# Performance work log

Hardware: AMD Instinct MI355X
Metric: run time of the kernel (lower is better)

The kernel has to match this reference:

```python
import jax, jax.numpy as jnp
import numpy as np

EPS = 1e-5

def layer_norm(x, g, b):
    mu = jnp.mean(x, axis=-1, keepdims=True)
    var = jnp.mean(jnp.square(x - mu), axis=-1, keepdims=True)
    return (x - mu) * jax.lax.rsqrt(var + EPS) * g + b

def setup_inputs() -> dict:
    key = jax.random.key(0)
    ks = jax.random.split(key, 8)
    B, N, C, H = 1, 384, 128, 128
    s = 0.02
    return {
        "pair": jax.random.normal(ks[0], (B, N, N, C), dtype=jnp.float32),
        "ln_l_g": jnp.ones((C,), jnp.float32), "ln_l_b": jnp.zeros((C,), jnp.float32),
        "ln_r_g": jnp.ones((C,), jnp.float32), "ln_r_b": jnp.zeros((C,), jnp.float32),
        "Wl": jax.random.normal(ks[1], (C, H), jnp.float32) * s, "bl": jnp.zeros((H,), jnp.float32),
        "Wr": jax.random.normal(ks[2], (C, H), jnp.float32) * s, "br": jnp.zeros((H,), jnp.float32),
        "Wg": jax.random.normal(ks[3], (C, H), jnp.float32) * s, "bg": jnp.zeros((H,), jnp.float32),
        "Wo": jax.random.normal(ks[4], (H, C), jnp.float32) * s, "bo": jnp.zeros((C,), jnp.float32),
        "n_g": jnp.ones((C,), jnp.float32), "n_b": jnp.zeros((C,), jnp.float32),
    }

def reference(pair, ln_l_g, ln_l_b, ln_r_g, ln_r_b, Wl, bl, Wr, br, Wg, bg, Wo, bo, n_g, n_b):
    # pair: [B, N, N, C]
    left = layer_norm(pair, ln_l_g, ln_l_b) @ Wl + bl      # [B,N,N,H]
    right = layer_norm(pair, ln_r_g, ln_r_b) @ Wr + br     # [B,N,N,H]
    gate = jax.nn.sigmoid(pair @ Wg + bg)                  # [B,N,N,H]
    # triangle multiplicative update: per-channel N x N matmul over k
    out = jnp.einsum('bikh,bkjh->bijh', left, right)
    out = out * gate
    out = out @ Wo + bo                                    # [B,N,N,C]
    return layer_norm(out + pair, n_g, n_b)
```

## Files before the change

### kernel.cpp

```cpp
#include <hip/hip_runtime.h>
#include <hip/hip_bf16.h>

#define N_ 384
#define C_ 128
#define M_ (N_*N_)

typedef __attribute__((ext_vector_type(8))) short bf16x8_t;
typedef __attribute__((ext_vector_type(4))) float f32x4_t;
typedef unsigned int u32;
typedef unsigned short u16;
typedef unsigned long long u64;

__device__ __forceinline__ u16 f2bf(float f) {
  u32 u = __builtin_bit_cast(u32, f);
  u32 r = (u + 0x7FFFu + ((u >> 16) & 1u)) >> 16;
  return (u16)r;
}
__device__ __forceinline__ float bf2f(u16 h) {
  u32 u = ((u32)h) << 16;
  return __builtin_bit_cast(float, u);
}

__global__ __launch_bounds__(256) void k_prep(const float* __restrict__ lg, const float* __restrict__ rg,
    const float* __restrict__ Wl, const float* __restrict__ Wr, const float* __restrict__ Wg,
    const float* __restrict__ Wo,
    const float* __restrict__ lb, const float* __restrict__ rb,
    const float* __restrict__ bl, const float* __restrict__ br, const float* __restrict__ bg,
    u16* __restrict__ wcat, u16* __restrict__ wot,
    float* __restrict__ bcat, float* __restrict__ sg) {
  int bx = blockIdx.x, t = threadIdx.x;
  if (bx < 256) {
    int idx = bx*256 + t;
    if (idx < 49152) {
      int n = idx >> 7, k = idx & 127;
      float v;
      if (n < 128)      v = lg[k] * Wl[k*128 + n];
      else if (n < 256) v = rg[k] * Wr[k*128 + (n-128)];
      else              v = Wg[k*128 + (n-256)];
      wcat[idx] = f2bf(v);
    } else {
      int i2 = idx - 49152;
      int c = i2 >> 7, h = i2 & 127;
      wot[i2] = f2bf(Wo[h*128 + c]);
    }
  } else if (bx == 256) {
    float s = 0.f;
    if (t < 128)      { for (int k=0;k<128;k++) s += lb[k]*Wl[k*128+t];       s += bl[t];     bcat[t] = s; }
    else              { int hh=t-128; for (int k=0;k<128;k++) s += rb[k]*Wr[k*128+hh]; s += br[hh]; bcat[t] = s; }
  } else {
    if (t < 128)      { bcat[256+t] = bg[t]; }
    else              { int hh = t-128; float s=0.f; for (int k=0;k<128;k++) s += Wg[k*128+hh]; sg[hh] = s; }
  }
}

#define LDK 136
#define LDA 72
#define LDW 72
#define LDT 136

__global__ __launch_bounds__(512) void k_projln(const float* __restrict__ pair,
    const u16* __restrict__ wcat, const float* __restrict__ bcat, const float* __restrict__ sg,
    u16* __restrict__ left_t, u16* __restrict__ right_t, u16* __restrict__ gate_t) {
  __shared__ u16 At[128*LDK];
  __shared__ float mu_s[128];
  __shared__ float irs_s[128];
  int bx = blockIdx.x;
  int r0 = bx * 128;
  int t = threadIdx.x, w = t>>6, lane = t&63;
  int q = lane>>4, nl = lane&15;

  {
    int rr = t >> 2, quarter = t & 3;
    const float4* gp = (const float4*)(pair + (size_t)(r0+rr)*128 + quarter*32);
    float4 v[8];
    #pragma unroll
    for (int i=0;i<8;i++) v[i] = gp[i];
    float s=0.f, qq=0.f;
    #pragma unroll
    for (int i=0;i<8;i++) {
      s  += v[i].x + v[i].y + v[i].z + v[i].w;
      qq += v[i].x*v[i].x + v[i].y*v[i].y + v[i].z*v[i].z + v[i].w*v[i].w;
    }
    s  += __shfl_xor(s, 1, 64);
    s  += __shfl_xor(s, 2, 64);
    qq += __shfl_xor(qq, 1, 64);
    qq += __shfl_xor(qq, 2, 64);
    float mu = s * (1.f/128.f);
    float var = qq*(1.f/128.f) - mu*mu;
    float rstd = rsqrtf(var + 1e-5f);
    if (quarter == 0) { mu_s[rr] = mu; irs_s[rr] = 1.0f/rstd; }
    u32* lp = (u32*)(At + rr*LDK + quarter*32);
    #pragma unroll
    for (int i=0;i<4;i++) {
      u32 p0 = (u32)f2bf((v[2*i].x-mu)*rstd)   | ((u32)f2bf((v[2*i].y-mu)*rstd)<<16);
      u32 p1 = (u32)f2bf((v[2*i].z-mu)*rstd)   | ((u32)f2bf((v[2*i].w-mu)*rstd)<<16);
      u32 p2 = (u32)f2bf((v[2*i+1].x-mu)*rstd) | ((u32)f2bf((v[2*i+1].y-mu)*rstd)<<16);
      u32 p3 = (u32)f2bf((v[2*i+1].z-mu)*rstd) | ((u32)f2bf((v[2*i+1].w-mu)*rstd)<<16);
      ((uint4*)lp)[i] = make_uint4(p0,p1,p2,p3);
    }
  }
  __syncthreads();

  #pragma unroll 1
  for (int nb = 0; nb < 3; ++nb) {
    const u16* bbase = wcat + (size_t)(nb*128)*128;
    f32x4_t acc[8] = {};
    #pragma unroll
    for (int ks=0; ks<4; ks++) {
      int kel = ks*32 + q*8;
      bf16x8_t b = *(const bf16x8_t*)(bbase + (size_t)(w*16 + nl)*128 + kel);
      #pragma unroll
      for (int tm=0;tm<8;tm++) {
        bf16x8_t a = *(const bf16x8_t*)(At + (tm*16+nl)*LDK + kel);
        acc[tm] = __builtin_amdgcn_mfma_f32_16x16x32_bf16(a, b, acc[tm], 0,0,0);
      }
    }
    u16* dst = (nb==0) ? left_t : (nb==1) ? right_t : gate_t;
    int n = w*16 + nl;
    float bias = bcat[nb*128 + n];
    u16* rowp = dst + (size_t)n*M_ + r0;
    if (nb == 2) {
      float sgn = sg[n];
      #pragma unroll
      for (int tm=0;tm<8;tm++) {
        f32x4_t mu4 = *(const f32x4_t*)(mu_s  + tm*16 + q*4);
        f32x4_t ir4 = *(const f32x4_t*)(irs_s + tm*16 + q*4);
        float v0 = acc[tm][0]*ir4[0] + mu4[0]*sgn + bias;
        float v1 = acc[tm][1]*ir4[1] + mu4[1]*sgn + bias;
        float v2 = acc[tm][2]*ir4[2] + mu4[2]*sgn + bias;
        float v3 = acc[tm][3]*ir4[3] + mu4[3]*sgn + bias;
        v0 = 1.0f/(1.0f+__expf(-v0));
        v1 = 1.0f/(1.0f+__expf(-v1));
        v2 = 1.0f/(1.0f+__expf(-v2));
        v3 = 1.0f/(1.0f+__expf(-v3));
        u32 pk0 = (u32)f2bf(v0) | ((u32)f2bf(v1)<<16);
        u32 pk1 = (u32)f2bf(v2) | ((u32)f2bf(v3)<<16);
        *(u64*)(rowp + tm*16 + q*4) = (u64)pk0 | ((u64)pk1<<32);
      }
    } else {
      #pragma unroll
      for (int tm=0;tm<8;tm++) {
        u32 pk0 = (u32)f2bf(acc[tm][0]+bias) | ((u32)f2bf(acc[tm][1]+bias)<<16);
        u32 pk1 = (u32)f2bf(acc[tm][2]+bias) | ((u32)f2bf(acc[tm][3]+bias)<<16);
        *(u64*)(rowp + tm*16 + q*4) = (u64)pk0 | ((u64)pk1<<32);
      }
    }
  }
}

__global__ __launch_bounds__(512) void k_einsum(const u16* __restrict__ left_t, const u16* __restrict__ right_t,
    const u16* __restrict__ gate_t, u16* __restrict__ og_t) {
  __shared__ u16 smem[2*128*LDA];
  u16* At = smem; u16* Bt = smem + 128*LDA;
  int bx = blockIdx.x;
  int wk = (bx & 7) * 144 + (bx >> 3);
  int h = wk / 9; int rem = wk % 9;
  int i0 = (rem/3)*128, j0 = (rem%3)*128;
  const u16* Ag = left_t + (size_t)h*M_;
  const u16* Bg = right_t + (size_t)h*M_;
  int t = threadIdx.x, w = t>>6, lane = t&63;
  int q = lane>>4, nl = lane&15;
  f32x4_t acc[4][2] = {};
  int m0 = (w&1)*64, nb0 = (w>>1)*32;
  for (int kb = 0; kb < N_; kb += 64) {
    {
      int rr = t>>2, quarter = t&3;
      const u16* gp = Ag + (size_t)(i0+rr)*N_ + kb + quarter*16;
      u16* lp = At + rr*LDA + quarter*16;
      ((uint4*)lp)[0] = ((const uint4*)gp)[0];
      ((uint4*)lp)[1] = ((const uint4*)gp)[1];
    }
    {
      int kk2 = t>>4;
      int seg = t&15;
      const u16* g0 = Bg + (size_t)(kb + 2*kk2)*N_ + j0 + seg*8;
      const u16* g1 = g0 + N_;
      uint4 ra = ((const uint4*)g0)[0];
      uint4 rbv = ((const uint4*)g1)[0];
      u32 w0[4] = {ra.x,ra.y,ra.z,ra.w};
      u32 w1[4] = {rbv.x,rbv.y,rbv.z,rbv.w};
      u32 sw = (u32)(seg>>1) << 4;
      char* bbytes = (char*)Bt;
      #pragma unroll
      for (int e=0;e<4;e++) {
        u32 lo = w0[e], hi = w1[e];
        u32 evenw = (lo & 0xffffu) | (hi << 16);
        u32 oddw  = (lo >> 16)     | (hi & 0xffff0000u);
        int je = seg*8 + 2*e;
        u32 byteE = ((u32)(je*LDA + 2*kk2) * 2u) ^ sw;
        u32 byteO = ((u32)((je+1)*LDA + 2*kk2) * 2u) ^ sw;
        *(u32*)(bbytes + byteE) = evenw;
        *(u32*)(bbytes + byteO) = oddw;
      }
    }
    __syncthreads();
    #pragma unroll
    for (int ks=0; ks<2; ks++) {
      int kel = ks*32 + q*8;
      bf16x8_t a[4], b[2];
      #pragma unroll
      for (int tm=0;tm<4;tm++) a[tm] = *(const bf16x8_t*)(At + (m0+tm*16+nl)*LDA + kel);
      #pragma unroll
      for (int tn=0;tn<2;tn++) {
        u32 swr = (u32)(((nb0>>4) + tn) & 7) << 4;
        b[tn] = *(const bf16x8_t*)((const char*)Bt + ((u32)(((nb0+tn*16+nl)*LDA + kel)*2) ^ swr));
      }
      #pragma unroll
      for (int tm=0;tm<4;tm++)
        #pragma unroll
        for (int tn=0;tn<2;tn++)
          acc[tm][tn] = __builtin_amdgcn_mfma_f32_16x16x32_bf16(a[tm], b[tn], acc[tm][tn], 0,0,0);
    }
    __syncthreads();
  }
  u16* Ot = smem;
  #pragma unroll
  for (int tm=0;tm<4;tm++)
    #pragma unroll
    for (int tn=0;tn<2;tn++)
      #pragma unroll
      for (int p=0;p<4;p++) {
        int m = m0 + tm*16 + q*4 + p;
        int n = nb0 + tn*16 + nl;
        Ot[m*LDT + n] = f2bf(acc[tm][tn][p]);
      }
  __syncthreads();
  {
    int m = t>>2, hq = t&3;
    size_t rbase = (size_t)h*M_ + (size_t)(i0+m)*N_ + j0 + hq*32;
    const uint4* gg = (const uint4*)(gate_t + rbase);
    const uint4* lo = (const uint4*)(Ot + m*LDT + hq*32);
    uint4* od = (uint4*)(og_t + rbase);
    #pragma unroll
    for (int i=0;i<4;i++) {
      uint4 gv = gg[i]; uint4 ov = lo[i];
      u32 ga[4] = {gv.x,gv.y,gv.z,gv.w};
      u32 oa[4] = {ov.x,ov.y,ov.z,ov.w};
      u32 ra2[4];
      #pragma unroll
      for (int e=0;e<4;e++) {
        float g0 = bf2f((u16)(ga[e]&0xffffu)), g1 = bf2f((u16)(ga[e]>>16));
        float o0 = bf2f((u16)(oa[e]&0xffffu)), o1 = bf2f((u16)(oa[e]>>16));
        ra2[e] = (u32)f2bf(o0*g0) | ((u32)f2bf(o1*g1)<<16);
      }
      od[i] = make_uint4(ra2[0],ra2[1],ra2[2],ra2[3]);
    }
  }
}

__global__ __launch_bounds__(512) void k_final(const u16* __restrict__ og_t, const u16* __restrict__ wot,
    const float* __restrict__ pair, const float* __restrict__ bo,
    const float* __restrict__ ng, const float* __restrict__ nb_,
    float* __restrict__ out) {
  __shared__ u16 smem[2*128*LDW];
  u16* At = smem; u16* Wt = smem + 128*LDW;
  int bx = blockIdx.x;
  int r0 = bx * 128;
  int t = threadIdx.x, w = t>>6, lane = t&63;
  int q = lane>>4, nl = lane&15;
  f32x4_t acc[8] = {};
  int m0 = w*16;
  for (int c0 = 0; c0 < 128; c0 += 64) {
    {
      int hh = t>>3, seg = t&7;
      const u16* gp = og_t + (size_t)(c0+hh)*M_ + r0 + seg*16;
      uint4 b0 = ((const uint4*)gp)[0];
      uint4 b1 = ((const uint4*)gp)[1];
      u32 xs[8] = {b0.x,b0.y,b0.z,b0.w,b1.x,b1.y,b1.z,b1.w};
      #pragma unroll
      for (int e=0;e<8;e++) {
        int rb = seg*16 + 2*e;
        At[(rb+0)*LDW+hh] = (u16)(xs[e]&0xffffu);
        At[(rb+1)*LDW+hh] = (u16)(xs[e]>>16);
      }
    }
    {
      int c = t>>2, q4 = t&3;
      const u16* gp = wot + (size_t)c*128 + c0 + q4*16;
      u16* lp = Wt + c*LDW + q4*16;
      ((uint4*)lp)[0] = ((const uint4*)gp)[0];
      ((uint4*)lp)[1] = ((const uint4*)gp)[1];
    }
    __syncthreads();
    #pragma unroll
    for (int ks=0; ks<2; ks++) {
      int kel = ks*32 + q*8;
      bf16x8_t a = *(const bf16x8_t*)(At + (m0+nl)*LDW + kel);
      bf16x8_t b[8];
      #pragma unroll
      for (int tn=0;tn<8;tn++) b[tn] = *(const bf16x8_t*)(Wt + (tn*16+nl)*LDW + kel);
      #pragma unroll
      for (int tn=0;tn<8;tn++)
        acc[tn] = __builtin_amdgcn_mfma_f32_16x16x32_bf16(a, b[tn], acc[tn], 0,0,0);
    }
    __syncthreads();
  }
  float rsum[4], rsq[4];
  #pragma unroll
  for (int p=0;p<4;p++) { rsum[p]=0.f; rsq[p]=0.f; }
  #pragma unroll
  for (int tn=0;tn<8;tn++) {
    int n = tn*16 + nl;
    float bb = bo[n];
    #pragma unroll
    for (int p=0;p<4;p++) {
      int m = m0 + q*4 + p;
      float v = acc[tn][p] + bb + pair[(size_t)(r0+m)*128 + n];
      acc[tn][p] = v;
      rsum[p] += v;
      rsq[p]  += v*v;
    }
  }
  #pragma unroll
  for (int msk=1; msk<16; msk<<=1) {
    #pragma unroll
    for (int p=0;p<4;p++) {
      rsum[p] += __shfl_xor(rsum[p], msk, 64);
      rsq[p]  += __shfl_xor(rsq[p],  msk, 64);
    }
  }
  #pragma unroll
  for (int p=0;p<4;p++) {
    float mu = rsum[p] * (1.f/128.f);
    float var = rsq[p]*(1.f/128.f) - mu*mu;
    rsum[p] = mu;
    rsq[p] = rsqrtf(var + 1e-5f);
  }
  #pragma unroll
  for (int tn=0;tn<8;tn++) {
    int n = tn*16 + nl;
    float g = ng[n], b2 = nb_[n];
    #pragma unroll
    for (int p=0;p<4;p++) {
      int m = m0 + q*4 + p;
      out[(size_t)(r0+m)*128 + n] = (acc[tn][p] - rsum[p]) * rsq[p] * g + b2;
    }
  }
}

extern "C" void kernel_launch(void* const* d_in, const int* in_sizes, int n_in,
                              void* d_out, int out_size, void* d_ws, size_t ws_size,
                              hipStream_t stream) {
  (void)in_sizes; (void)n_in; (void)out_size; (void)ws_size;
  const float* pair   = (const float*)d_in[0];
  const float* ln_l_g = (const float*)d_in[1];
  const float* ln_l_b = (const float*)d_in[2];
  const float* ln_r_g = (const float*)d_in[3];
  const float* ln_r_b = (const float*)d_in[4];
  const float* Wl = (const float*)d_in[5];
  const float* bl = (const float*)d_in[6];
  const float* Wr = (const float*)d_in[7];
  const float* br = (const float*)d_in[8];
  const float* Wg = (const float*)d_in[9];
  const float* bg = (const float*)d_in[10];
  const float* Wo = (const float*)d_in[11];
  const float* bo = (const float*)d_in[12];
  const float* n_g = (const float*)d_in[13];
  const float* n_b = (const float*)d_in[14];

  char* ws = (char*)d_ws;
  const size_t SZ = (size_t)M_*128*sizeof(u16);
  u16*  og_t    = (u16*)(ws);
  u16*  gate_t  = (u16*)(ws + SZ);
  u16*  wcat    = (u16*)(ws + 2*SZ);
  float* bcat   = (float*)(ws + 2*SZ + 98304);
  float* sgp    = (float*)(ws + 2*SZ + 98304 + 1536);
  u16*  wot     = (u16*)(ws + 2*SZ + 98304 + 1536 + 512);

  u16* left_t   = (u16*)d_out;
  u16* right_t  = (u16*)d_out + (size_t)M_*128;

  k_prep<<<258, 256, 0, stream>>>(ln_l_g, ln_r_g, Wl, Wr, Wg, Wo,
                                  ln_l_b, ln_r_b, bl, br, bg, wcat, wot, bcat, sgp);
  k_projln<<<1152, 512, 0, stream>>>(pair, wcat, bcat, sgp, left_t, right_t, gate_t);
  k_einsum<<<1152, 512, 0, stream>>>(left_t, right_t, gate_t, og_t);
  k_final<<<1152, 512, 0, stream>>>(og_t, wot, pair, bo, n_g, n_b, (float*)d_out);
}
```

Baseline: 271.4 us.

## Store intermediates as 128x128 tiles so each block's writes and reads are contiguous

Left/right, gate and gated-output intermediates change from a channel-major [H][N*N] layout to a tiled layout. Left and right blocks of one 128-row tile are interleaved together, and each 128-row by 128-channel tile is stored contiguously. Projection and final kernels now write and read one contiguous 32KB region per block instead of 128 strided rows spread across M. The einsum kernel reads 256-byte segments from scattered tiles instead of contiguous rows, so its access locality may suffer.

```diff
diff --git a/kernel.cpp b/kernel.cpp
--- a/kernel.cpp
+++ b/kernel.cpp
@@ -60,7 +60,7 @@
 
 __global__ __launch_bounds__(512) void k_projln(const float* __restrict__ pair,
     const u16* __restrict__ wcat, const float* __restrict__ bcat, const float* __restrict__ sg,
-    u16* __restrict__ left_t, u16* __restrict__ right_t, u16* __restrict__ gate_t) {
+    u16* __restrict__ lr_, u16* __restrict__ gate_) {
   __shared__ u16 At[128*LDK];
   __shared__ float mu_s[128];
   __shared__ float irs_s[128];
@@ -115,10 +115,12 @@
         acc[tm] = __builtin_amdgcn_mfma_f32_16x16x32_bf16(a, b, acc[tm], 0,0,0);
       }
     }
-    u16* dst = (nb==0) ? left_t : (nb==1) ? right_t : gate_t;
     int n = w*16 + nl;
     float bias = bcat[nb*128 + n];
-    u16* rowp = dst + (size_t)n*M_ + r0;
+    u16* rowp;
+    if (nb == 0)      rowp = lr_   + ((size_t)bx*256 + n)*128;
+    else if (nb == 1) rowp = lr_   + ((size_t)bx*256 + 128 + n)*128;
+    else              rowp = gate_ + ((size_t)bx*128 + n)*128;
     if (nb == 2) {
       float sgn = sg[n];
       #pragma unroll
@@ -148,24 +150,23 @@
   }
 }
 
-__global__ __launch_bounds__(512) void k_einsum(const u16* __restrict__ left_t, const u16* __restrict__ right_t,
-    const u16* __restrict__ gate_t, u16* __restrict__ og_t) {
+__global__ __launch_bounds__(512) void k_einsum(const u16* __restrict__ lr_,
+    const u16* __restrict__ gate_, u16* __restrict__ og_) {
   __shared__ u16 smem[2*128*LDA];
   u16* At = smem; u16* Bt = smem + 128*LDA;
   int bx = blockIdx.x;
   int wk = (bx & 7) * 144 + (bx >> 3);
   int h = wk / 9; int rem = wk % 9;
-  int i0 = (rem/3)*128, j0 = (rem%3)*128;
-  const u16* Ag = left_t + (size_t)h*M_;
-  const u16* Bg = right_t + (size_t)h*M_;
+  int i0 = (rem/3)*128, j0c = rem%3;
   int t = threadIdx.x, w = t>>6, lane = t&63;
   int q = lane>>4, nl = lane&15;
   f32x4_t acc[4][2] = {};
   int m0 = (w&1)*64, nb0 = (w>>1)*32;
   for (int kb = 0; kb < N_; kb += 64) {
+    int c = kb >> 7, off = kb & 127;
     {
       int rr = t>>2, quarter = t&3;
-      const u16* gp = Ag + (size_t)(i0+rr)*N_ + kb + quarter*16;
+      const u16* gp = lr_ + (((size_t)(i0+rr)*3 + c)*256 + h)*128 + off + quarter*16;
       u16* lp = At + rr*LDA + quarter*16;
       ((uint4*)lp)[0] = ((const uint4*)gp)[0];
       ((uint4*)lp)[1] = ((const uint4*)gp)[1];
@@ -173,8 +174,8 @@
     {
       int kk2 = t>>4;
       int seg = t&15;
-      const u16* g0 = Bg + (size_t)(kb + 2*kk2)*N_ + j0 + seg*8;
-      const u16* g1 = g0 + N_;
+      const u16* g0 = lr_ + (((size_t)(kb + 2*kk2)*3 + j0c)*256 + 128 + h)*128 + seg*8;
+      const u16* g1 = g0 + 3*256*128;
       uint4 ra = ((const uint4*)g0)[0];
       uint4 rbv = ((const uint4*)g1)[0];
       u32 w0[4] = {ra.x,ra.y,ra.z,ra.w};
@@ -227,10 +228,10 @@
   __syncthreads();
   {
     int m = t>>2, hq = t&3;
-    size_t rbase = (size_t)h*M_ + (size_t)(i0+m)*N_ + j0 + hq*32;
-    const uint4* gg = (const uint4*)(gate_t + rbase);
+    size_t gbase = (((size_t)(i0+m)*3 + j0c)*128 + h)*128 + hq*32;
+    const uint4* gg = (const uint4*)(gate_ + gbase);
     const uint4* lo = (const uint4*)(Ot + m*LDT + hq*32);
-    uint4* od = (uint4*)(og_t + rbase);
+    uint4* od = (uint4*)(og_ + gbase);
     #pragma unroll
     for (int i=0;i<4;i++) {
       uint4 gv = gg[i]; uint4 ov = lo[i];
@@ -248,7 +249,7 @@
   }
 }
 
-__global__ __launch_bounds__(512) void k_final(const u16* __restrict__ og_t, const u16* __restrict__ wot,
+__global__ __launch_bounds__(512) void k_final(const u16* __restrict__ og_, const u16* __restrict__ wot,
     const float* __restrict__ pair, const float* __restrict__ bo,
     const float* __restrict__ ng, const float* __restrict__ nb_,
     float* __restrict__ out) {
@@ -263,7 +264,7 @@
   for (int c0 = 0; c0 < 128; c0 += 64) {
     {
       int hh = t>>3, seg = t&7;
-      const u16* gp = og_t + (size_t)(c0+hh)*M_ + r0 + seg*16;
+      const u16* gp = og_ + ((size_t)bx*128 + (c0+hh))*128 + seg*16;
       uint4 b0 = ((const uint4*)gp)[0];
       uint4 b1 = ((const uint4*)gp)[1];
       u32 xs[8] = {b0.x,b0.y,b0.z,b0.w,b1.x,b1.y,b1.z,b1.w};
@@ -360,19 +361,18 @@
 
   char* ws = (char*)d_ws;
   const size_t SZ = (size_t)M_*128*sizeof(u16);
-  u16*  og_t    = (u16*)(ws);
-  u16*  gate_t  = (u16*)(ws + SZ);
-  u16*  wcat    = (u16*)(ws + 2*SZ);
-  float* bcat   = (float*)(ws + 2*SZ + 98304);
-  float* sgp    = (float*)(ws + 2*SZ + 98304 + 1536);
-  u16*  wot     = (u16*)(ws + 2*SZ + 98304 + 1536 + 512);
-
-  u16* left_t   = (u16*)d_out;
-  u16* right_t  = (u16*)d_out + (size_t)M_*128;
+  u16*  og    = (u16*)(ws);
+  u16*  gate  = (u16*)(ws + SZ);
+  u16*  wcat  = (u16*)(ws + 2*SZ);
+  float* bcat = (float*)(ws + 2*SZ + 98304);
+  float* sgp  = (float*)(ws + 2*SZ + 98304 + 1536);
+  u16*  wot   = (u16*)(ws + 2*SZ + 98304 + 1536 + 512);
+
+  u16* lr = (u16*)d_out;
 
   k_prep<<<258, 256, 0, stream>>>(ln_l_g, ln_r_g, Wl, Wr, Wg, Wo,
                                   ln_l_b, ln_r_b, bl, br, bg, wcat, wot, bcat, sgp);
-  k_projln<<<1152, 512, 0, stream>>>(pair, wcat, bcat, sgp, left_t, right_t, gate_t);
-  k_einsum<<<1152, 512, 0, stream>>>(left_t, right_t, gate_t, og_t);
-  k_final<<<1152, 512, 0, stream>>>(og_t, wot, pair, bo, n_g, n_b, (float*)d_out);
-}
+  k_projln<<<1152, 512, 0, stream>>>(pair, wcat, bcat, sgp, lr, gate);
+  k_einsum<<<1152, 512, 0, stream>>>(lr, gate, og);
+  k_final<<<1152, 512, 0, stream>>>(og, wot, pair, bo, n_g, n_b, (float*)d_out);
+}
```

Result: no change. 268.9 us (-0.9%).
